# Performance work log

Hardware: AMD Instinct MI355X
Metric: run time of the kernel (lower is better)

Reference implementation:

```python
import jax, jax.numpy as jnp
import numpy as np

B, T, V, D = 64, 2048, 32000, 256  # batch, seq_len, vocab, emb_dim == hidden_size
H = D
NUM_CLASSES = 27
N_NODES = 128


def setup_inputs() -> dict:
    key = jax.random.key(0)
    ks = jax.random.split(key, 8)
    s = 1.0 / np.sqrt(D)
    return {
        "tokens": jax.random.randint(ks[0], (B, T), 0, V),
        "node_token_span_starts": jax.random.randint(ks[1], (B, N_NODES), 0, T),
        "node_token_span_ends": jax.random.randint(ks[2], (B, N_NODES), 0, T),
        "embed": jax.random.normal(ks[3], (V, D), dtype=jnp.float32),
        "Wi": jax.random.normal(ks[4], (D, 4 * H), dtype=jnp.float32) * s,
        "Wh": jax.random.normal(ks[5], (H, 4 * H), dtype=jnp.float32) * s,
        "bh": jnp.zeros((4 * H,), dtype=jnp.float32),
        "Wo": jax.random.normal(ks[6], (H, NUM_CLASSES), dtype=jnp.float32) * s,
        "bo": jnp.zeros((NUM_CLASSES,), dtype=jnp.float32),
    }


def reference(tokens, node_token_span_starts, node_token_span_ends,
              embed, Wi, Wh, bh, Wo, bo):
    # node_token_span_* are unused by the original forward (dead code).
    x = embed[tokens.astype(jnp.int32)]            # [B, T, D]
    # Precompute input projections for all timesteps in one big GEMM.
    zx = jnp.einsum('btd,df->btf', x, Wi) + bh     # [B, T, 4H]
    batch = tokens.shape[0]
    c0 = jnp.zeros((batch, H), dtype=x.dtype)
    h0 = jnp.zeros((batch, H), dtype=x.dtype)

    def step(carry, zxt):
        c, h = carry
        z = zxt + h @ Wh                           # [B, 4H]
        i, f, g, o = jnp.split(z, 4, axis=-1)
        c = jax.nn.sigmoid(f) * c + jax.nn.sigmoid(i) * jnp.tanh(g)
        h = jax.nn.sigmoid(o) * jnp.tanh(c)
        return (c, h), h

    (c, h), _ = jax.lax.scan(step, (c0, h0), jnp.swapaxes(zx, 0, 1))
    # forward_outputs[:, -1, :] == final hidden state h
    return h @ Wo + bo                             # [B, NUM_CLASSES]
```

## Files before the change

kernel.cpp:

```cpp
#include <hip/hip_runtime.h>
#include <hip/hip_bf16.h>
#include <stdint.h>

typedef __hip_bfloat16 bf16;
typedef __attribute__((ext_vector_type(8))) short short8;
typedef __attribute__((ext_vector_type(4))) float f32x4;
typedef __attribute__((ext_vector_type(4))) int i32x4;
typedef __attribute__((ext_vector_type(4))) unsigned int u32x4;

#define NB   64
#define NT   2048
#define NV   32000
#define ND   256
#define NH4  1024
#define NCLS 27


__global__ __launch_bounds__(256) void k_cvt_embed(const float* __restrict__ e,
                                                   bf16* __restrict__ o) {
  int i = blockIdx.x * blockDim.x + threadIdx.x;
  float4 v = reinterpret_cast<const float4*>(e)[i];
  union { bf16 h[4]; uint2 u; } pk;
  pk.h[0] = __float2bfloat16(v.x);
  pk.h[1] = __float2bfloat16(v.y);
  pk.h[2] = __float2bfloat16(v.z);
  pk.h[3] = __float2bfloat16(v.w);
  reinterpret_cast<uint2*>(o)[i] = pk.u;
}

__global__ __launch_bounds__(256) void k_cvt_wi(const float* __restrict__ wi,
                                                bf16* __restrict__ wit) {
  int i = blockIdx.x * blockDim.x + threadIdx.x;
  int col = i >> 8;
  int k   = i & 255;
  wit[i] = __float2bfloat16(wi[k * NH4 + col]);
}

__global__ __launch_bounds__(256) void k_scale(const float* __restrict__ wh,
                                               float* __restrict__ dq,
                                               float* __restrict__ rdq,
                                               float* __restrict__ rw) {
  int col = blockIdx.x * 256 + threadIdx.x;
  float m = 0.f;
  for (int k = 0; k < ND; ++k) m = fmaxf(m, fabsf(wh[k * NH4 + col]));
  dq[col]  = m * (1.f / 16129.f);
  rdq[col] = 16129.f / m;
  rw[col]  = 127.f / m;
}

__global__ __launch_bounds__(256) void k_cvt_whq(const float* __restrict__ wh,
                                                 const float* __restrict__ rw,
                                                 signed char* __restrict__ whq) {
  int idx  = blockIdx.x * 256 + threadIdx.x;
  int ii   = idx & 15;
  int lane = (idx >> 4) & 63;
  int kq   = (idx >> 10) & 3;
  int nt   = idx >> 12;
  int k   = kq * 64 + (lane >> 4) * 16 + ii;
  int col = nt * 16 + (lane & 15);
  whq[idx] = (signed char)(int)rintf(wh[k * NH4 + col] * rw[col]);
}

__global__ __launch_bounds__(256) void k_gemm_zx(const int*  __restrict__ tokens,
                                                 const bf16* __restrict__ eb,
                                                 const bf16* __restrict__ wit,
                                                 const float* __restrict__ rdq,
                                                 int* __restrict__ zxq,
                                                 int t0, int lgch) {
  __shared__ bf16 As[4 * 64 * 8];
  __shared__ bf16 Bs[4 * 64 * 8];
  int bid  = blockIdx.x;
  int nb   = bid & 15;
  int mb   = bid >> 4;
  int n0   = nb * 64;
  int tid  = threadIdx.x, lane = tid & 63, wave = tid >> 6;
  int wm   = wave >> 1, wn = wave & 1;
  int srow = tid >> 2;
  int skg  = tid & 3;

  long trow = (long)tokens[srow * NT + t0 + mb] * ND;
  const bf16* ap = eb  + trow + skg * 8;
  const bf16* bp = wit + (long)(n0 + srow) * ND + skg * 8;
  bf16* as_dst = &As[(skg * 64 + srow) * 8];
  bf16* bs_dst = &Bs[(skg * 64 + srow) * 8];

  f32x4 acc[2][2] = {};
  for (int k0 = 0; k0 < ND; k0 += 32) {
    __syncthreads();
    *(u32x4*)as_dst = *(const u32x4*)(ap + k0);
    *(u32x4*)bs_dst = *(const u32x4*)(bp + k0);
    __syncthreads();
    short8 a0 = *(const short8*)&As[((lane >> 4) * 64 + wm * 32 +  0 + (lane & 15)) * 8];
    short8 a1 = *(const short8*)&As[((lane >> 4) * 64 + wm * 32 + 16 + (lane & 15)) * 8];
    short8 b0 = *(const short8*)&Bs[((lane >> 4) * 64 + wn * 32 +  0 + (lane & 15)) * 8];
    short8 b1 = *(const short8*)&Bs[((lane >> 4) * 64 + wn * 32 + 16 + (lane & 15)) * 8];
    acc[0][0] = __builtin_amdgcn_mfma_f32_16x16x32_bf16(a0, b0, acc[0][0], 0, 0, 0);
    acc[0][1] = __builtin_amdgcn_mfma_f32_16x16x32_bf16(a0, b1, acc[0][1], 0, 0, 0);
    acc[1][0] = __builtin_amdgcn_mfma_f32_16x16x32_bf16(a1, b0, acc[1][0], 0, 0, 0);
    acc[1][1] = __builtin_amdgcn_mfma_f32_16x16x32_bf16(a1, b1, acc[1][1], 0, 0, 0);
  }

  int cb  = n0 + wn * 32 + (lane & 15);
  float rq0 = rdq[cb], rq1 = rdq[cb + 16];
  int bb = wm * 32 + (lane >> 4) * 4;
#pragma unroll
  for (int fm = 0; fm < 2; ++fm) {
#pragma unroll
    for (int fn = 0; fn < 2; ++fn) {
      int col = cb + fn * 16;
      int uu  = col & 255, q = col >> 8;
      float rq = fn ? rq1 : rq0;
#pragma unroll
      for (int i2 = 0; i2 < 4; ++i2) {
        int rr = bb + fm * 16 + i2;
        int p0 = rr >> 1;
        size_t idx = (((size_t)(p0 << lgch) + mb) * 2 + (rr & 1)) * 1024 + uu * 4 + q;
        zxq[idx] = (int)rintf(acc[fm][fn][i2] * rq);
      }
    }
  }
}

__device__ __forceinline__ float sigf(float x) {
  return __builtin_amdgcn_rcpf(1.f + __expf(-x));
}
__device__ __forceinline__ float tanh_fast(float x) {
  return 1.f - 2.f * __builtin_amdgcn_rcpf(1.f + __expf(2.f * x));
}

#define LSTM_STEP(ZX, ST)                                                       \
  {                                                                             \
    i32x4 a0 = *(const i32x4*)&aF[0 * 1024 + l * 16];                           \
    i32x4 a1 = *(const i32x4*)&aF[1 * 1024 + l * 16];                           \
    i32x4 a2 = *(const i32x4*)&aF[2 * 1024 + l * 16];                           \
    i32x4 a3 = *(const i32x4*)&aF[3 * 1024 + l * 16];                           \
    i32x4 acc[8];                                                               \
    _Pragma("unroll")                                                           \
    for (int j = 0; j < 8; ++j) {                                               \
      i32x4 t;                                                                  \
      t = __builtin_amdgcn_mfma_i32_16x16x64_i8(a0, w[j][0], czero, 0, 0, 0);   \
      t = __builtin_amdgcn_mfma_i32_16x16x64_i8(a1, w[j][1], t, 0, 0, 0);       \
      t = __builtin_amdgcn_mfma_i32_16x16x64_i8(a2, w[j][2], t, 0, 0, 0);       \
      acc[j] = __builtin_amdgcn_mfma_i32_16x16x64_i8(a3, w[j][3], t, 0, 0, 0);  \
    }                                                                           \
    if (l4 == 0) {                                                              \
      _Pragma("unroll")                                                         \
      for (int j = 0; j < 8; ++j) {                                             \
        int col = (wv * 8 + j) * 16 + l15;                                      \
        int tt  = ((col & 255) << 2) | (col >> 8);                              \
        zl[tt]        = acc[j][0];                                              \
        zl[1024 + tt] = acc[j][1];                                              \
      }                                                                         \
    }                                                                           \
    __syncthreads();                                                            \
    {                                                                           \
      i32x4 zr = *(const i32x4*)&zl[b * 1024 + u * 4];                          \
      int s0 = zr[0] + ZX[0];                                                   \
      int s1 = zr[1] + ZX[1];                                                   \
      int s2 = zr[2] + ZX[2];                                                   \
      int s3 = zr[3] + ZX[3];                                                   \
      if ((ST) + 2 < tn)                                                        \
        ZX = *(const i32x4*)(zg + (size_t)((ST) + 2) * 2048);                   \
      float zi = (float)s0 * dqv[0] + bhv[0];                                   \
      float zf = (float)s1 * dqv[1] + bhv[1];                                   \
      float zg_ = (float)s2 * dqv[2] + bhv[2];                                  \
      float zo = (float)s3 * dqv[3] + bhv[3];                                   \
      c = sigf(zf) * c + sigf(zi) * tanh_fast(zg_);                             \
      float h = sigf(zo) * tanh_fast(c);                                        \
      aF[kqu * 1024 + (b | (lgu << 4)) * 16 + iiu] =                            \
          (signed char)(int)rintf(h * 127.f);                                   \
      if ((ST) == tn - 1) hst[(p * 2 + b) * 256 + u] = h;                       \
    }                                                                           \
    __syncthreads();                                                            \
  }

__global__ __launch_bounds__(512, 1) void k_lstm(const int* __restrict__ zxq,
                                                 const signed char* __restrict__ whq,
                                                 const float* __restrict__ dq,
                                                 const float* __restrict__ bh,
                                                 float* __restrict__ cst,
                                                 float* __restrict__ hst,
                                                 int t0, int tn, int lgch) {
  __shared__ int  zl[2 * 1024];
  __shared__ signed char aF[4 * 64 * 16];

  int p   = blockIdx.x;
  int tid = threadIdx.x;
  int l   = tid & 63;
  int wv  = tid >> 6;
  int l15 = l & 15, l4 = l >> 4;
  int u   = tid & 255;
  int b   = tid >> 8;

  i32x4 w[8][4];
#pragma unroll
  for (int j = 0; j < 8; ++j) {
    int nt = wv * 8 + j;
#pragma unroll
    for (int kq = 0; kq < 4; ++kq)
      w[j][kq] = *(const i32x4*)&whq[((nt * 4 + kq) * 64 + l) * 16];
  }
#pragma unroll
  for (int j = 0; j < 8; ++j)
#pragma unroll
    for (int kq = 0; kq < 4; ++kq)
      asm volatile("" : "+v"(w[j][kq]));

  i32x4 czero = (i32x4)0;
  asm volatile("" : "+v"(czero));

  float dqv[4], bhv[4];
#pragma unroll
  for (int q = 0; q < 4; ++q) { dqv[q] = dq[q * 256 + u]; bhv[q] = bh[q * 256 + u]; }
  float c = (t0 == 0) ? 0.f : cst[(p * 2 + b) * 256 + u];

  int kqu = u >> 6, lgu = (u >> 4) & 3, iiu = u & 15;

  if (tid < 256) ((i32x4*)aF)[tid] = (i32x4)0;
  __syncthreads();
  if (t0 != 0) {
    int hq = (int)rintf(hst[(p * 2 + b) * 256 + u] * 127.f);
    aF[kqu * 1024 + (b | (lgu << 4)) * 16 + iiu] = (signed char)hq;
  }
  __syncthreads();

  const int* zg = zxq + ((size_t)(p << lgch) * 2 + b) * 1024 + u * 4;
  i32x4 zxA = *(const i32x4*)zg;
  i32x4 zxB = *(const i32x4*)(zg + 2048);

  for (int lt = 0; lt < tn; lt += 2) {
    LSTM_STEP(zxA, lt)
    LSTM_STEP(zxB, lt + 1)
  }

  cst[(p * 2 + b) * 256 + u] = c;
}

__global__ __launch_bounds__(64) void k_out(const float* __restrict__ hfin,
                                            const float* __restrict__ wo,
                                            const float* __restrict__ bo,
                                            float* __restrict__ y) {
  __shared__ float hsm[256];
  int b = blockIdx.x, tid = threadIdx.x;
  for (int i = tid; i < 256; i += 64) hsm[i] = hfin[b * 256 + i];
  __syncthreads();
  if (tid < NCLS) {
    float s = bo[tid];
    for (int k = 0; k < 256; ++k) s += hsm[k] * wo[k * NCLS + tid];
    y[b * NCLS + tid] = s;
  }
}

extern "C" void kernel_launch(void* const* d_in, const int* in_sizes, int n_in,
                              void* d_out, int out_size, void* d_ws, size_t ws_size,
                              hipStream_t stream) {
  const int*   tokens = (const int*)d_in[0];
  const float* embed  = (const float*)d_in[3];
  const float* wi     = (const float*)d_in[4];
  const float* wh     = (const float*)d_in[5];
  const float* bh     = (const float*)d_in[6];
  const float* wo     = (const float*)d_in[7];
  const float* bo     = (const float*)d_in[8];
  float* y = (float*)d_out;

  char* ws = (char*)d_ws;
  bf16* eb        = (bf16*)ws;        ws += (size_t)NV * ND * 2;
  bf16* wit       = (bf16*)ws;        ws += (size_t)NH4 * ND * 2;
  signed char* whq = (signed char*)ws; ws += (size_t)ND * NH4;
  float* dqv      = (float*)ws;       ws += (size_t)NH4 * 4;
  float* rdq      = (float*)ws;       ws += (size_t)NH4 * 4;
  float* rw       = (float*)ws;       ws += (size_t)NH4 * 4;
  float* cst      = (float*)ws;       ws += (size_t)NB * ND * 4;
  float* hst      = (float*)ws;       ws += (size_t)NB * ND * 4;
  size_t fixed = (size_t)(ws - (char*)d_ws);

  int CHUNK = 32, lgch = 5;
  static const int cand[]  = {512, 256, 128, 64, 32};
  static const int candl[] = {9, 8, 7, 6, 5};
  for (int ci = 0; ci < 5; ++ci) {
    size_t need = fixed + (size_t)cand[ci] * 262144;
    if (need <= ws_size) { CHUNK = cand[ci]; lgch = candl[ci]; break; }
  }
  int* zxq = (int*)ws;

  hipLaunchKernelGGL(k_cvt_embed, dim3(NV * ND / 4 / 256), dim3(256), 0, stream, embed, eb);
  hipLaunchKernelGGL(k_cvt_wi,    dim3(NH4 * ND / 256), dim3(256), 0, stream, wi, wit);
  hipLaunchKernelGGL(k_scale,     dim3(4), dim3(256), 0, stream, wh, dqv, rdq, rw);
  hipLaunchKernelGGL(k_cvt_whq,   dim3(1024), dim3(256), 0, stream, wh, rw, whq);

  for (int t0 = 0; t0 < NT; t0 += CHUNK) {
    hipLaunchKernelGGL(k_gemm_zx, dim3(CHUNK * 16), dim3(256), 0, stream,
                       tokens, eb, wit, rdq, zxq, t0, lgch);
    hipLaunchKernelGGL(k_lstm, dim3(32), dim3(512), 0, stream,
                       zxq, whq, dqv, bh, cst, hst, t0, CHUNK, lgch);
  }
  hipLaunchKernelGGL(k_out, dim3(NB), dim3(64), 0, stream, hst, wo, bo, y);
}
```

Baseline: 2.229 ms.

## Overlap input-projection GEMM of next chunk with LSTM recurrence of current chunk

Merges the zx GEMM and the LSTM recurrence into one launch per chunk. Blocks 0-31 run the recurrence for chunk L-1 while 128 other blocks compute the input projections for chunk L into a double-buffered workspace. The GEMM's time is meant to hide behind the latency-bound serial recurrence, and the number of launches drops. The chunk size is now fixed at 256, so the workspace needs room for two 256-step buffers, and the GEMM blocks share the GPU with the recurrence blocks.

```diff
diff --git a/kernel.cpp b/kernel.cpp
--- a/kernel.cpp
+++ b/kernel.cpp
@@ -14,6 +14,8 @@
 #define ND   256
 #define NH4  1024
 #define NCLS 27
+#define CH   256
+#define NCH  (NT / CH)
 
 
 __global__ __launch_bounds__(256) void k_cvt_embed(const float* __restrict__ e,
@@ -59,66 +61,6 @@
   int k   = kq * 64 + (lane >> 4) * 16 + ii;
   int col = nt * 16 + (lane & 15);
   whq[idx] = (signed char)(int)rintf(wh[k * NH4 + col] * rw[col]);
-}
-
-__global__ __launch_bounds__(256) void k_gemm_zx(const int*  __restrict__ tokens,
-                                                 const bf16* __restrict__ eb,
-                                                 const bf16* __restrict__ wit,
-                                                 const float* __restrict__ rdq,
-                                                 int* __restrict__ zxq,
-                                                 int t0, int lgch) {
-  __shared__ bf16 As[4 * 64 * 8];
-  __shared__ bf16 Bs[4 * 64 * 8];
-  int bid  = blockIdx.x;
-  int nb   = bid & 15;
-  int mb   = bid >> 4;
-  int n0   = nb * 64;
-  int tid  = threadIdx.x, lane = tid & 63, wave = tid >> 6;
-  int wm   = wave >> 1, wn = wave & 1;
-  int srow = tid >> 2;
-  int skg  = tid & 3;
-
-  long trow = (long)tokens[srow * NT + t0 + mb] * ND;
-  const bf16* ap = eb  + trow + skg * 8;
-  const bf16* bp = wit + (long)(n0 + srow) * ND + skg * 8;
-  bf16* as_dst = &As[(skg * 64 + srow) * 8];
-  bf16* bs_dst = &Bs[(skg * 64 + srow) * 8];
-
-  f32x4 acc[2][2] = {};
-  for (int k0 = 0; k0 < ND; k0 += 32) {
-    __syncthreads();
-    *(u32x4*)as_dst = *(const u32x4*)(ap + k0);
-    *(u32x4*)bs_dst = *(const u32x4*)(bp + k0);
-    __syncthreads();
-    short8 a0 = *(const short8*)&As[((lane >> 4) * 64 + wm * 32 +  0 + (lane & 15)) * 8];
-    short8 a1 = *(const short8*)&As[((lane >> 4) * 64 + wm * 32 + 16 + (lane & 15)) * 8];
-    short8 b0 = *(const short8*)&Bs[((lane >> 4) * 64 + wn * 32 +  0 + (lane & 15)) * 8];
-    short8 b1 = *(const short8*)&Bs[((lane >> 4) * 64 + wn * 32 + 16 + (lane & 15)) * 8];
-    acc[0][0] = __builtin_amdgcn_mfma_f32_16x16x32_bf16(a0, b0, acc[0][0], 0, 0, 0);
-    acc[0][1] = __builtin_amdgcn_mfma_f32_16x16x32_bf16(a0, b1, acc[0][1], 0, 0, 0);
-    acc[1][0] = __builtin_amdgcn_mfma_f32_16x16x32_bf16(a1, b0, acc[1][0], 0, 0, 0);
-    acc[1][1] = __builtin_amdgcn_mfma_f32_16x16x32_bf16(a1, b1, acc[1][1], 0, 0, 0);
-  }
-
-  int cb  = n0 + wn * 32 + (lane & 15);
-  float rq0 = rdq[cb], rq1 = rdq[cb + 16];
-  int bb = wm * 32 + (lane >> 4) * 4;
-#pragma unroll
-  for (int fm = 0; fm < 2; ++fm) {
-#pragma unroll
-    for (int fn = 0; fn < 2; ++fn) {
-      int col = cb + fn * 16;
-      int uu  = col & 255, q = col >> 8;
-      float rq = fn ? rq1 : rq0;
-#pragma unroll
-      for (int i2 = 0; i2 < 4; ++i2) {
-        int rr = bb + fm * 16 + i2;
-        int p0 = rr >> 1;
-        size_t idx = (((size_t)(p0 << lgch) + mb) * 2 + (rr & 1)) * 1024 + uu * 4 + q;
-        zxq[idx] = (int)rintf(acc[fm][fn][i2] * rq);
-      }
-    }
-  }
 }
 
 __device__ __forceinline__ float sigf(float x) {
@@ -159,7 +101,7 @@
       int s1 = zr[1] + ZX[1];                                                   \
       int s2 = zr[2] + ZX[2];                                                   \
       int s3 = zr[3] + ZX[3];                                                   \
-      if ((ST) + 2 < tn)                                                        \
+      if ((ST) + 2 < CH)                                                        \
         ZX = *(const i32x4*)(zg + (size_t)((ST) + 2) * 2048);                   \
       float zi = (float)s0 * dqv[0] + bhv[0];                                   \
       float zf = (float)s1 * dqv[1] + bhv[1];                                   \
@@ -169,71 +111,147 @@
       float h = sigf(zo) * tanh_fast(c);                                        \
       aF[kqu * 1024 + (b | (lgu << 4)) * 16 + iiu] =                            \
           (signed char)(int)rintf(h * 127.f);                                   \
-      if ((ST) == tn - 1) hst[(p * 2 + b) * 256 + u] = h;                       \
+      if ((ST) == CH - 1) hst[(p * 2 + b) * 256 + u] = h;                       \
     }                                                                           \
     __syncthreads();                                                            \
   }
 
-__global__ __launch_bounds__(512, 1) void k_lstm(const int* __restrict__ zxq,
-                                                 const signed char* __restrict__ whq,
-                                                 const float* __restrict__ dq,
-                                                 const float* __restrict__ bh,
-                                                 float* __restrict__ cst,
-                                                 float* __restrict__ hst,
-                                                 int t0, int tn, int lgch) {
-  __shared__ int  zl[2 * 1024];
-  __shared__ signed char aF[4 * 64 * 16];
-
-  int p   = blockIdx.x;
-  int tid = threadIdx.x;
-  int l   = tid & 63;
-  int wv  = tid >> 6;
-  int l15 = l & 15, l4 = l >> 4;
-  int u   = tid & 255;
-  int b   = tid >> 8;
-
-  i32x4 w[8][4];
-#pragma unroll
-  for (int j = 0; j < 8; ++j) {
-    int nt = wv * 8 + j;
-#pragma unroll
-    for (int kq = 0; kq < 4; ++kq)
-      w[j][kq] = *(const i32x4*)&whq[((nt * 4 + kq) * 64 + l) * 16];
+__global__ __launch_bounds__(512, 1) void k_fused(const int*  __restrict__ tokens,
+                                                  const bf16* __restrict__ eb,
+                                                  const bf16* __restrict__ wit,
+                                                  const float* __restrict__ rdq,
+                                                  const signed char* __restrict__ whq,
+                                                  const float* __restrict__ dq,
+                                                  const float* __restrict__ bh,
+                                                  float* __restrict__ cst,
+                                                  float* __restrict__ hst,
+                                                  int* __restrict__ zxqA,
+                                                  int* __restrict__ zxqB,
+                                                  int L) {
+  __shared__ char smem[16384];
+  int bid = blockIdx.x;
+
+  if (bid < 32) {
+    if (L == 0) return;
+    int* zl = (int*)smem;
+    signed char* aF = (signed char*)(smem + 8192);
+    const int* __restrict__ zxq = ((L - 1) & 1) ? zxqB : zxqA;
+    int t0 = (L - 1) * CH;
+
+    int p   = bid;
+    int tid = threadIdx.x;
+    int l   = tid & 63;
+    int wv  = tid >> 6;
+    int l15 = l & 15, l4 = l >> 4;
+    int u   = tid & 255;
+    int b   = tid >> 8;
+
+    i32x4 w[8][4];
+#pragma unroll
+    for (int j = 0; j < 8; ++j) {
+      int nt = wv * 8 + j;
+#pragma unroll
+      for (int kq = 0; kq < 4; ++kq)
+        w[j][kq] = *(const i32x4*)&whq[((nt * 4 + kq) * 64 + l) * 16];
+    }
+#pragma unroll
+    for (int j = 0; j < 8; ++j)
+#pragma unroll
+      for (int kq = 0; kq < 4; ++kq)
+        asm volatile("" : "+v"(w[j][kq]));
+
+    i32x4 czero = (i32x4)0;
+    asm volatile("" : "+v"(czero));
+
+    float dqv[4], bhv[4];
+#pragma unroll
+    for (int q = 0; q < 4; ++q) { dqv[q] = dq[q * 256 + u]; bhv[q] = bh[q * 256 + u]; }
+    float c = (t0 == 0) ? 0.f : cst[(p * 2 + b) * 256 + u];
+
+    int kqu = u >> 6, lgu = (u >> 4) & 3, iiu = u & 15;
+
+    if (tid < 256) ((i32x4*)aF)[tid] = (i32x4)0;
+    __syncthreads();
+    if (t0 != 0) {
+      int hq = (int)rintf(hst[(p * 2 + b) * 256 + u] * 127.f);
+      aF[kqu * 1024 + (b | (lgu << 4)) * 16 + iiu] = (signed char)hq;
+    }
+    __syncthreads();
+
+    const int* zg = zxq + ((size_t)(p * CH) * 2 + b) * 1024 + u * 4;
+    i32x4 zxA = *(const i32x4*)zg;
+    i32x4 zxB = *(const i32x4*)(zg + 2048);
+
+    for (int lt = 0; lt < CH; lt += 2) {
+      LSTM_STEP(zxA, lt)
+      LSTM_STEP(zxB, lt + 1)
+    }
+
+    cst[(p * 2 + b) * 256 + u] = c;
+
+  } else {
+    if (L >= NCH) return;
+    int* __restrict__ zxw = (L & 1) ? zxqB : zxqA;
+    int t0 = L * CH;
+    int hh   = threadIdx.x >> 8;
+    int tid2 = threadIdx.x & 255;
+    bf16* As = (bf16*)(smem + hh * 8192);
+    bf16* Bs = (bf16*)(smem + hh * 8192 + 4096);
+
+    int lane = tid2 & 63, wave = tid2 >> 6;
+    int wm   = wave >> 1, wn = wave & 1;
+    int srow = tid2 >> 2;
+    int skg  = tid2 & 3;
+    bf16* as_dst = &As[(skg * 64 + srow) * 8];
+    bf16* bs_dst = &Bs[(skg * 64 + srow) * 8];
+
+    for (int it = 0; it < 16; ++it) {
+      int tg = ((bid - 32) + it * 128) * 2 + hh;
+      int mb = tg >> 4;
+      int nb = tg & 15;
+      int n0 = nb * 64;
+
+      long trow = (long)tokens[srow * NT + t0 + mb] * ND;
+      const bf16* ap = eb  + trow + skg * 8;
+      const bf16* bp = wit + (long)(n0 + srow) * ND + skg * 8;
+
+      f32x4 acc[2][2] = {};
+      for (int k0 = 0; k0 < ND; k0 += 32) {
+        __syncthreads();
+        *(u32x4*)as_dst = *(const u32x4*)(ap + k0);
+        *(u32x4*)bs_dst = *(const u32x4*)(bp + k0);
+        __syncthreads();
+        short8 a0 = *(const short8*)&As[((lane >> 4) * 64 + wm * 32 +  0 + (lane & 15)) * 8];
+        short8 a1 = *(const short8*)&As[((lane >> 4) * 64 + wm * 32 + 16 + (lane & 15)) * 8];
+        short8 b0 = *(const short8*)&Bs[((lane >> 4) * 64 + wn * 32 +  0 + (lane & 15)) * 8];
+        short8 b1 = *(const short8*)&Bs[((lane >> 4) * 64 + wn * 32 + 16 + (lane & 15)) * 8];
+        acc[0][0] = __builtin_amdgcn_mfma_f32_16x16x32_bf16(a0, b0, acc[0][0], 0, 0, 0);
+        acc[0][1] = __builtin_amdgcn_mfma_f32_16x16x32_bf16(a0, b1, acc[0][1], 0, 0, 0);
+        acc[1][0] = __builtin_amdgcn_mfma_f32_16x16x32_bf16(a1, b0, acc[1][0], 0, 0, 0);
+        acc[1][1] = __builtin_amdgcn_mfma_f32_16x16x32_bf16(a1, b1, acc[1][1], 0, 0, 0);
+      }
+
+      int cb  = n0 + wn * 32 + (lane & 15);
+      float rq0 = rdq[cb], rq1 = rdq[cb + 16];
+      int bb = wm * 32 + (lane >> 4) * 4;
+#pragma unroll
+      for (int fm = 0; fm < 2; ++fm) {
+#pragma unroll
+        for (int fn = 0; fn < 2; ++fn) {
+          int col = cb + fn * 16;
+          int uu  = col & 255, q = col >> 8;
+          float rq = fn ? rq1 : rq0;
+#pragma unroll
+          for (int i2 = 0; i2 < 4; ++i2) {
+            int rr = bb + fm * 16 + i2;
+            int p0 = rr >> 1;
+            size_t idx = (((size_t)(p0 * CH) + mb) * 2 + (rr & 1)) * 1024 + uu * 4 + q;
+            zxw[idx] = (int)rintf(acc[fm][fn][i2] * rq);
+          }
+        }
+      }
+    }
   }
-#pragma unroll
-  for (int j = 0; j < 8; ++j)
-#pragma unroll
-    for (int kq = 0; kq < 4; ++kq)
-      asm volatile("" : "+v"(w[j][kq]));
-
-  i32x4 czero = (i32x4)0;
-  asm volatile("" : "+v"(czero));
-
-  float dqv[4], bhv[4];
-#pragma unroll
-  for (int q = 0; q < 4; ++q) { dqv[q] = dq[q * 256 + u]; bhv[q] = bh[q * 256 + u]; }
-  float c = (t0 == 0) ? 0.f : cst[(p * 2 + b) * 256 + u];
-
-  int kqu = u >> 6, lgu = (u >> 4) & 3, iiu = u & 15;
-
-  if (tid < 256) ((i32x4*)aF)[tid] = (i32x4)0;
-  __syncthreads();
-  if (t0 != 0) {
-    int hq = (int)rintf(hst[(p * 2 + b) * 256 + u] * 127.f);
-    aF[kqu * 1024 + (b | (lgu << 4)) * 16 + iiu] = (signed char)hq;
-  }
-  __syncthreads();
-
-  const int* zg = zxq + ((size_t)(p << lgch) * 2 + b) * 1024 + u * 4;
-  i32x4 zxA = *(const i32x4*)zg;
-  i32x4 zxB = *(const i32x4*)(zg + 2048);
-
-  for (int lt = 0; lt < tn; lt += 2) {
-    LSTM_STEP(zxA, lt)
-    LSTM_STEP(zxB, lt + 1)
-  }
-
-  cst[(p * 2 + b) * 256 + u] = c;
 }
 
 __global__ __launch_bounds__(64) void k_out(const float* __restrict__ hfin,
@@ -264,35 +282,26 @@
   float* y = (float*)d_out;
 
   char* ws = (char*)d_ws;
-  bf16* eb        = (bf16*)ws;        ws += (size_t)NV * ND * 2;
-  bf16* wit       = (bf16*)ws;        ws += (size_t)NH4 * ND * 2;
+  bf16* eb         = (bf16*)ws;        ws += (size_t)NV * ND * 2;
+  bf16* wit        = (bf16*)ws;        ws += (size_t)NH4 * ND * 2;
   signed char* whq = (signed char*)ws; ws += (size_t)ND * NH4;
-  float* dqv      = (float*)ws;       ws += (size_t)NH4 * 4;
-  float* rdq      = (float*)ws;       ws += (size_t)NH4 * 4;
-  float* rw       = (float*)ws;       ws += (size_t)NH4 * 4;
-  float* cst      = (float*)ws;       ws += (size_t)NB * ND * 4;
-  float* hst      = (float*)ws;       ws += (size_t)NB * ND * 4;
-  size_t fixed = (size_t)(ws - (char*)d_ws);
-
-  int CHUNK = 32, lgch = 5;
-  static const int cand[]  = {512, 256, 128, 64, 32};
-  static const int candl[] = {9, 8, 7, 6, 5};
-  for (int ci = 0; ci < 5; ++ci) {
-    size_t need = fixed + (size_t)cand[ci] * 262144;
-    if (need <= ws_size) { CHUNK = cand[ci]; lgch = candl[ci]; break; }
-  }
-  int* zxq = (int*)ws;
+  float* dqv       = (float*)ws;       ws += (size_t)NH4 * 4;
+  float* rdq       = (float*)ws;       ws += (size_t)NH4 * 4;
+  float* rw        = (float*)ws;       ws += (size_t)NH4 * 4;
+  float* cst       = (float*)ws;       ws += (size_t)NB * ND * 4;
+  float* hst       = (float*)ws;       ws += (size_t)NB * ND * 4;
+  int* zxqA        = (int*)ws;         ws += (size_t)CH * 262144;
+  int* zxqB        = (int*)ws;         ws += (size_t)CH * 262144;
 
   hipLaunchKernelGGL(k_cvt_embed, dim3(NV * ND / 4 / 256), dim3(256), 0, stream, embed, eb);
   hipLaunchKernelGGL(k_cvt_wi,    dim3(NH4 * ND / 256), dim3(256), 0, stream, wi, wit);
   hipLaunchKernelGGL(k_scale,     dim3(4), dim3(256), 0, stream, wh, dqv, rdq, rw);
   hipLaunchKernelGGL(k_cvt_whq,   dim3(1024), dim3(256), 0, stream, wh, rw, whq);
 
-  for (int t0 = 0; t0 < NT; t0 += CHUNK) {
-    hipLaunchKernelGGL(k_gemm_zx, dim3(CHUNK * 16), dim3(256), 0, stream,
-                       tokens, eb, wit, rdq, zxq, t0, lgch);
-    hipLaunchKernelGGL(k_lstm, dim3(32), dim3(512), 0, stream,
-                       zxq, whq, dqv, bh, cst, hst, t0, CHUNK, lgch);
+  for (int L = 0; L <= NCH; ++L) {
+    hipLaunchKernelGGL(k_fused, dim3(160), dim3(512), 0, stream,
+                       tokens, eb, wit, rdq, whq, dqv, bh, cst, hst,
+                       zxqA, zxqB, L);
   }
   hipLaunchKernelGGL(k_out, dim3(NB), dim3(64), 0, stream, hst, wo, bo, y);
 }
```

Measured after the change: 2.161 ms (median of 2 runs). 1.03x faster.
